# Kernel tuning notes

Hardware: AMD Instinct MI355X
Metric: run time of the kernel (lower is better)

The kernel has to match this reference:

```python
import jax, jax.numpy as jnp
import numpy as np

B, C, T = 32, 64, 512
K = 3            # period_channels / top-k frequencies
PMAX = T         # max period (== seq_len so output matches input length)
MIN_P = 32       # min_period_threshold
CMAX = T // MIN_P  # static upper bound on number of cycles
KERNELS = ((1, 1), (3, 3), (5, 5))


def _conv2d(x, w, b, pad):
    # x: [N, Cin, H, W], w: [Cout, Cin, kh, kw]
    y = jax.lax.conv_general_dilated(
        x, w, (1, 1), ((pad[0], pad[0]), (pad[1], pad[1])),
        dimension_numbers=('NCHW', 'OIHW', 'NCHW'))
    return y + b[None, :, None, None]


def _period_fold(seqs):
    # seqs: [BN, T]. FFT top-k period detection + gather-based fold into 2D grids.
    spec = jnp.fft.rfft(seqs, axis=-1)
    amp = jnp.abs(spec).at[..., 0].set(0.0)  # zero DC component
    vals, idx = jax.lax.top_k(amp, K)        # [BN, K]
    idx = jnp.maximum(idx, 1)
    P = jnp.clip(T // idx, MIN_P, PMAX)      # period length per branch
    cycles = jnp.maximum(T // P, 1)
    base = jnp.maximum(T - cycles * P, 0)    # start offset (keep trailing window)
    idx_c = jnp.arange(CMAX)
    idx_p = jnp.arange(PMAX)
    gidx = (base[:, :, None, None]
            + idx_c[None, None, :, None] * P[:, :, None, None]
            + idx_p[None, None, None, :])
    gidx = jnp.clip(gidx, 0, T - 1)          # [BN, K, CMAX, PMAX]
    gathered = seqs[jnp.arange(seqs.shape[0])[:, None, None, None], gidx]
    mask = ((idx_c[None, None, :, None] < cycles[:, :, None, None])
            & (idx_p[None, None, None, :] < P[:, :, None, None])).astype(seqs.dtype)
    return gathered * mask, mask, vals


def _forward(features, w_path0, b_path0, w_path1, b_path1, w_path2, b_path2,
             w_proj, b_proj, w_res, b_res, w_fuse, b_fuse):
    seqs = features.reshape(B * C, T)
    conv_in, mask, kamp = _period_fold(seqs)  # [B*C, K, CMAX, PMAX]
    # Inception block: parallel same-padded convs + 1x1 proj + residual 1x1 proj
    ws = (w_path0, w_path1, w_path2)
    bs = (b_path0, b_path1, b_path2)
    feats = [_conv2d(conv_in, w, b, (kh // 2, kw // 2))
             for w, b, (kh, kw) in zip(ws, bs, KERNELS)]
    z = _conv2d(jnp.concatenate(feats, axis=1), w_proj, b_proj, (0, 0))
    z = jax.nn.gelu(z, approximate=False)  # torch nn.GELU default = exact erf
    z2d = (z + _conv2d(conv_in, w_res, b_res, (0, 0))).reshape(B, C, CMAX, PMAX)
    mask5 = mask.reshape(B, C, K, CMAX, PMAX)
    conv_in5 = conv_in.reshape(B, C, K, CMAX, PMAX)
    eps = jnp.finfo(z2d.dtype).eps
    neg = jnp.finfo(z2d.dtype).min
    # masked avg / max pooling over cycles
    cycle_mask = mask5.max(axis=2)                       # [B,C,CMAX,PMAX]
    avg_pool = (z2d * cycle_mask).sum(axis=2) / (cycle_mask.sum(axis=2) + eps)
    valid = cycle_mask > 0
    max_pool = jnp.where(valid, z2d, neg).max(axis=2)
    max_pool = jnp.where(valid.any(axis=2), max_pool, 0.0)  # [B,C,PMAX]
    # amplitude-softmax weighted branch reconstruction back to 1D
    branch_sum = conv_in5.sum(axis=3)                    # [B,C,K,PMAX]
    branch_w = mask5.sum(axis=3)
    branch_recon = branch_sum / (branch_w + eps) * (branch_w > 0)
    branch_valid = mask5.max(axis=(3, 4)) > 0            # [B,C,K]
    amp = jnp.where(branch_valid, kamp.reshape(B, C, K), neg)
    bw = jax.nn.softmax(amp, axis=2) * branch_valid
    seq_recon = (branch_recon * bw[..., None]).sum(axis=2)  # [B,C,PMAX]
    combined = jnp.concatenate([avg_pool, max_pool, seq_recon], axis=1)  # [B,3C,PMAX]
    fused = jnp.einsum('oc,bct->bot', w_fuse, combined) + b_fuse[None, :, None]
    return jax.nn.gelu(fused, approximate=False)  # [B, C, T] residual update


def setup_inputs() -> dict:
    key = jax.random.key(0)
    ks = jax.random.split(key, 8)

    def conv_w(k, shape):
        fan_in = shape[1] * shape[2] * shape[3]
        return jax.random.normal(k, shape, jnp.float32) / float(np.sqrt(fan_in))

    inp = {'features': jax.random.normal(ks[0], (B, C, T), jnp.float32)}
    for i, (kh, kw) in enumerate(KERNELS):
        inp[f'w_path{i}'] = conv_w(ks[1 + i], (1, K, kh, kw))
        inp[f'b_path{i}'] = jnp.zeros((1,), jnp.float32)
    inp['w_proj'] = conv_w(ks[4], (1, len(KERNELS), 1, 1))
    inp['b_proj'] = jnp.zeros((1,), jnp.float32)
    inp['w_res'] = conv_w(ks[5], (1, K, 1, 1))
    inp['b_res'] = jnp.zeros((1,), jnp.float32)
    inp['w_fuse'] = jax.random.normal(ks[6], (C, 3 * C), jnp.float32) / float(np.sqrt(3 * C))
    inp['b_fuse'] = jnp.zeros((C,), jnp.float32)
    return inp


def reference(features, w_path0, b_path0, w_path1, b_path1, w_path2, b_path2,
              w_proj, b_proj, w_res, b_res, w_fuse, b_fuse):
    return _forward(features, w_path0, b_path0, w_path1, b_path1, w_path2, b_path2,
                    w_proj, b_proj, w_res, b_res, w_fuse, b_fuse)
```

## Files before the change

### kernel.cpp

```cpp
#include <hip/hip_runtime.h>
#include <math.h>

#define B_    32
#define C_    64
#define T_    512
#define NROWS (B_ * C_)
#define CMAX_ 16
#define FEPS  1.1920929e-07f

__device__ __forceinline__ float gelu_fast(float x) {
    float y = fmaf(0.044715f * x * x, x, x);
    float e = __builtin_exp2f(-2.3022808f * y);
    return x * __builtin_amdgcn_rcpf(1.0f + e);
}

__global__ __launch_bounds__(128) void mono_kernel(
    const float* __restrict__ feat,
    const float* __restrict__ w0, const float* __restrict__ b0,
    const float* __restrict__ w1, const float* __restrict__ b1,
    const float* __restrict__ w2, const float* __restrict__ b2,
    const float* __restrict__ wpj, const float* __restrict__ bpj,
    const float* __restrict__ wr, const float* __restrict__ br,
    float* __restrict__ avg_out, float* __restrict__ max_out,
    float* __restrict__ seq_out)
{
    __shared__ float rowp[1040];
    __shared__ __align__(16) float2 FA[256];
    __shared__ __align__(16) float2 FB[256];
    __shared__ float WeffS[80];
    __shared__ float wtopS[6];
    __shared__ int   itopS[6];
    __shared__ int   ipS[9];
    __shared__ float bwS[3];

    const int tid = threadIdx.x;
    const int r = blockIdx.x;

    {
        float4 v = reinterpret_cast<const float4*>(feat + (size_t)r * T_)[tid];
        int bi = 2 + tid * 4;
        rowp[bi + 0] = v.x; rowp[bi + 1] = v.y;
        rowp[bi + 2] = v.z; rowp[bi + 3] = v.w;
    }
    for (int i = 514 + tid; i < 1040; i += 128) rowp[i] = 0.f;
    if (tid == 0) { rowp[0] = 0.f; rowp[1] = 0.f; }
    if (tid < 80) {
        int i = tid;
        if (i < 75) {
            int k = i / 25, ij = i % 25, ii = ij / 5, jj = ij % 5;
            float w = wpj[2] * w2[k * 25 + ii * 5 + jj];
            if (ii >= 1 && ii <= 3 && jj >= 1 && jj <= 3)
                w += wpj[1] * w1[k * 9 + (ii - 1) * 3 + (jj - 1)];
            if (ii == 2 && jj == 2) w += wpj[0] * w0[k];
            WeffS[i] = w;
        } else if (i == 75) {
            WeffS[75] = wpj[0] * b0[0] + wpj[1] * b1[0] + wpj[2] * b2[0] + bpj[0];
        } else if (i <= 78) {
            WeffS[i] = wr[i - 76];
        } else {
            WeffS[79] = br[0];
        }
    }
    __syncthreads();

    FA[tid]       = make_float2(rowp[2 + 2 * tid],         rowp[2 + 2 * tid + 1]);
    FA[tid + 128] = make_float2(rowp[2 + 2 * (tid + 128)], rowp[2 + 2 * (tid + 128) + 1]);
    __syncthreads();

    {
        float2* src = FA;
        float2* dst = FB;
        #pragma unroll
        for (int s = 1; s <= 8; ++s) {
            const int l = 1 << (s - 1);
            const int p = tid & (l - 1);
            const int i0 = 2 * tid - p;
            const float rev = (float)p * (0.5f / (float)l);
            const float cw =  __builtin_amdgcn_cosf(rev);
            const float sw = -__builtin_amdgcn_sinf(rev);
            float2 a = src[tid];
            float2 b = src[tid + 128];
            float tr = cw * b.x - sw * b.y;
            float ti = cw * b.y + sw * b.x;
            dst[i0]     = make_float2(a.x + tr, a.y + ti);
            dst[i0 + l] = make_float2(a.x - tr, a.y - ti);
            __syncthreads();
            float2* tmp = src; src = dst; dst = tmp;
        }
    }

    float v[2]; int id[2];
    #pragma unroll
    for (int q = 0; q < 2; ++q) {
        const int k = 1 + tid + 128 * q;
        float2 A  = FA[k & 255];
        float2 Bv = FA[(256 - k) & 255];
        float Er = 0.5f * (A.x + Bv.x);
        float Ei = 0.5f * (A.y - Bv.y);
        float Or = 0.5f * (A.y + Bv.y);
        float Oi = 0.5f * (Bv.x - A.x);
        const float rev = (float)k * (1.0f / 512.0f);
        float sth = __builtin_amdgcn_sinf(rev);
        float cth = __builtin_amdgcn_cosf(rev);
        float Fr = Er + cth * Or + sth * Oi;
        float Fi = Ei + cth * Oi - sth * Or;
        v[q] = sqrtf(Fr * Fr + Fi * Fi);
        id[q] = k;
    }

    {
        const int wv = tid >> 6;
        float vals[3]; int idxs[3];
        #pragma unroll
        for (int kk = 0; kk < 3; ++kk) {
            float bv = v[0]; int bi = id[0];
            if (v[1] > bv || (v[1] == bv && id[1] < bi)) { bv = v[1]; bi = id[1]; }
            #pragma unroll
            for (int off = 32; off >= 1; off >>= 1) {
                float ov = __shfl_xor(bv, off, 64);
                int   oi = __shfl_xor(bi, off, 64);
                if (ov > bv || (ov == bv && oi < bi)) { bv = ov; bi = oi; }
            }
            vals[kk] = bv; idxs[kk] = bi;
            #pragma unroll
            for (int q = 0; q < 2; ++q)
                if (id[q] == bi) v[q] = -1e30f;
        }
        if ((tid & 63) == 0) {
            #pragma unroll
            for (int kk = 0; kk < 3; ++kk) {
                wtopS[wv * 3 + kk] = vals[kk];
                itopS[wv * 3 + kk] = idxs[kk];
            }
        }
    }
    __syncthreads();
    if (tid == 0) {
        float vv[6]; int ii[6];
        #pragma unroll
        for (int q = 0; q < 6; ++q) { vv[q] = wtopS[q]; ii[q] = itopS[q]; }
        float vals[3]; int idxs[3];
        #pragma unroll
        for (int kk = 0; kk < 3; ++kk) {
            float bv = vv[0]; int bi = ii[0];
            #pragma unroll
            for (int q = 1; q < 6; ++q)
                if (vv[q] > bv || (vv[q] == bv && ii[q] < bi)) { bv = vv[q]; bi = ii[q]; }
            vals[kk] = bv; idxs[kk] = bi;
            #pragma unroll
            for (int q = 0; q < 6; ++q)
                if (ii[q] == bi) vv[q] = -1e30f;
        }
        float m = fmaxf(vals[0], fmaxf(vals[1], vals[2]));
        float e0 = expf(vals[0] - m), e1 = expf(vals[1] - m), e2 = expf(vals[2] - m);
        float inv = 1.0f / (e0 + e1 + e2);
        bwS[0] = e0 * inv; bwS[1] = e1 * inv; bwS[2] = e2 * inv;
        #pragma unroll
        for (int kk = 0; kk < 3; ++kk) {
            int fi = idxs[kk];
            int P = T_ / fi;
            P = P < 32 ? 32 : (P > 512 ? 512 : P);
            int cyc = T_ / P;
            ipS[kk] = P; ipS[3 + kk] = cyc; ipS[6 + kk] = T_ - cyc * P;
        }
    }
    __syncthreads();

    const int P0  = __builtin_amdgcn_readfirstlane(ipS[0]);
    const int P1  = __builtin_amdgcn_readfirstlane(ipS[1]);
    const int P2  = __builtin_amdgcn_readfirstlane(ipS[2]);
    const int cy0 = __builtin_amdgcn_readfirstlane(ipS[3]);
    const int cy1 = __builtin_amdgcn_readfirstlane(ipS[4]);
    const int cy2 = __builtin_amdgcn_readfirstlane(ipS[5]);
    const int bs0 = __builtin_amdgcn_readfirstlane(ipS[6]);
    const int bs1 = __builtin_amdgcn_readfirstlane(ipS[7]);
    const int bs2 = __builtin_amdgcn_readfirstlane(ipS[8]);
    const float bw0 = bwS[0], bw1 = bwS[1], bw2 = bwS[2];
    const float beff = WeffS[75], wr0 = WeffS[76], wr1 = WeffS[77],
                wr2 = WeffS[78], bres = WeffS[79];

    int maxP = P0 > P1 ? P0 : P1; maxP = maxP > P2 ? maxP : P2;
    const int PkA[3]  = {P0, P1, P2};
    const int cykA[3] = {cy0, cy1, cy2};
    const int bskA[3] = {bs0, bs1, bs2};
    const int woff = tid & 64;

    #pragma unroll 1
    for (int pc = 0; pc < T_; pc += 128) {
        const int p = pc + tid;
        const int wb = __builtin_amdgcn_readfirstlane(pc + woff);
        if (wb >= maxP) {
            avg_out[r * T_ + p] = 0.f;
            max_out[r * T_ + p] = 0.f;
            seq_out[r * T_ + p] = 0.f;
            continue;
        }
        int c0 = (P0 > wb) ? cy0 : 0;
        int c1 = (P1 > wb) ? cy1 : 0;
        int c2 = (P2 > wb) ? cy2 : 0;
        int cymax = c0 > c1 ? c0 : c1; cymax = cymax > c2 ? cymax : c2;
        cymax = __builtin_amdgcn_readfirstlane(cymax);

        float zacc[CMAX_];
        #pragma unroll
        for (int i = 0; i < CMAX_; ++i) zacc[i] = beff;

        #pragma unroll 1
        for (int k = 0; k < 3; ++k) {
            const int P = PkA[k];
            if (wb >= P) continue;
            const int cy = cykA[k];
            const int bs = bskA[k];
            float Wk[5][5];
            #pragma unroll
            for (int i = 0; i < 5; ++i)
                #pragma unroll
                for (int j = 0; j < 5; ++j)
                    Wk[i][j] = WeffS[k * 25 + i * 5 + j];
            bool mdw[5];
            #pragma unroll
            for (int dw = -2; dw <= 2; ++dw)
                mdw[dw + 2] = ((unsigned)(p + dw) < (unsigned)P);
            const int base = bs + p;
            float cur[5], nxt[5];
            #pragma unroll
            for (int dw = 0; dw < 5; ++dw) { cur[dw] = rowp[base + dw]; nxt[dw] = 0.f; }
            #pragma unroll
            for (int hh = 0; hh < CMAX_; ++hh) {
                if (hh < cy) {
                    if (hh + 1 < cy) {
                        const int a = base + (hh + 1) * P;
                        #pragma unroll
                        for (int dw = 0; dw < 5; ++dw) nxt[dw] = rowp[a + dw];
                    }
                    float w[5];
                    #pragma unroll
                    for (int dw = 0; dw < 5; ++dw) w[dw] = mdw[dw] ? cur[dw] : 0.f;
                    #pragma unroll
                    for (int dh = -2; dh <= 2; ++dh) {
                        const int cc = hh - dh;
                        if (cc >= 0 && cc < CMAX_) {
                            #pragma unroll
                            for (int dw = 0; dw < 5; ++dw)
                                zacc[cc] = fmaf(Wk[dh + 2][dw], w[dw], zacc[cc]);
                        }
                    }
                    #pragma unroll
                    for (int dw = 0; dw < 5; ++dw) cur[dw] = nxt[dw];
                }
            }
        }

        float avg_num = 0.f, den = 0.f, mx = -3.402823466e38f;
        float s0 = 0.f, s1 = 0.f, s2 = 0.f;
        int anyv = 0;
        const int pl0 = (p < P0), pl1 = (p < P1), pl2 = (p < P2);
        #pragma unroll
        for (int cc = 0; cc < CMAX_; ++cc) {
            if (cc < cymax) {
                int m0 = (cc < cy0) & pl0;
                int m1 = (cc < cy1) & pl1;
                int m2 = (cc < cy2) & pl2;
                float x0v = m0 ? rowp[2 + bs0 + cc * P0 + p] : 0.f;
                float x1v = m1 ? rowp[2 + bs1 + cc * P1 + p] : 0.f;
                float x2v = m2 ? rowp[2 + bs2 + cc * P2 + p] : 0.f;
                float res = fmaf(wr0, x0v, fmaf(wr1, x1v, fmaf(wr2, x2v, bres)));
                float z = gelu_fast(zacc[cc]) + res;
                s0 += x0v; s1 += x1v; s2 += x2v;
                int mm = m0 | m1 | m2;
                float cm = mm ? 1.f : 0.f;
                avg_num += z * cm;
                den += cm;
                mx = mm ? fmaxf(mx, z) : mx;
                anyv |= mm;
            }
        }
        float avg = avg_num / (den + FEPS);
        float mpool = anyv ? mx : 0.f;

        float seq = 0.f;
        seq = fmaf(bw0, pl0 ? s0 / ((float)cy0 + FEPS) : 0.f, seq);
        seq = fmaf(bw1, pl1 ? s1 / ((float)cy1 + FEPS) : 0.f, seq);
        seq = fmaf(bw2, pl2 ? s2 / ((float)cy2 + FEPS) : 0.f, seq);

        avg_out[r * T_ + p] = avg;
        max_out[r * T_ + p] = mpool;
        seq_out[r * T_ + p] = seq;
    }
}

__global__ __launch_bounds__(256) void fuse_kernel(
    const float* __restrict__ avgb, const float* __restrict__ maxb,
    const float* __restrict__ seqb,
    const float* __restrict__ wf, const float* __restrict__ bfu,
    float* __restrict__ out)
{
    __shared__ float wT[64][70];
    __shared__ float Bt[64][40];
    const int tid = threadIdx.x;
    const int b = blockIdx.y;
    const int tt0 = blockIdx.x * 32;
    const int og = tid >> 3;
    const int tg = tid & 7;
    const int o0 = og * 2;
    const int t0 = tg * 4;

    float acc[2][4];
    #pragma unroll
    for (int i = 0; i < 2; ++i)
        #pragma unroll
        for (int j = 0; j < 4; ++j) acc[i][j] = 0.f;

    const float* srcs[3] = {avgb, maxb, seqb};
    for (int g = 0; g < 3; ++g) {
        const float* __restrict__ src = srcs[g];
        #pragma unroll
        for (int it = 0; it < 2; ++it) {
            int idx = tid + it * 256;
            int c = idx >> 3, t4 = idx & 7;
            float4 vv = reinterpret_cast<const float4*>(
                            &src[(b * 64 + c) * 512 + tt0])[t4];
            *reinterpret_cast<float4*>(&Bt[c][t4 * 4]) = vv;
        }
        #pragma unroll
        for (int it = 0; it < 16; ++it) {
            int i = tid + it * 256;
            int c = i & 63, o = i >> 6;
            wT[c][o] = wf[o * 192 + g * 64 + c];
        }
        __syncthreads();
        for (int c = 0; c < 64; ++c) {
            float2 wv = *reinterpret_cast<const float2*>(&wT[c][o0]);
            float4 bv = *reinterpret_cast<const float4*>(&Bt[c][t0]);
            const float wa[2] = {wv.x, wv.y};
            const float ba[4] = {bv.x, bv.y, bv.z, bv.w};
            #pragma unroll
            for (int i = 0; i < 2; ++i)
                #pragma unroll
                for (int j = 0; j < 4; ++j)
                    acc[i][j] = fmaf(wa[i], ba[j], acc[i][j]);
        }
        __syncthreads();
    }
    #pragma unroll
    for (int i = 0; i < 2; ++i) {
        float bias = bfu[o0 + i];
        float4 o4;
        o4.x = gelu_fast(acc[i][0] + bias);
        o4.y = gelu_fast(acc[i][1] + bias);
        o4.z = gelu_fast(acc[i][2] + bias);
        o4.w = gelu_fast(acc[i][3] + bias);
        *reinterpret_cast<float4*>(
            &out[(b * 64 + (o0 + i)) * 512 + tt0 + t0]) = o4;
    }
}

extern "C" void kernel_launch(void* const* d_in, const int* in_sizes, int n_in,
                              void* d_out, int out_size, void* d_ws, size_t ws_size,
                              hipStream_t stream) {
    const float* feat = (const float*)d_in[0];
    const float* w0  = (const float*)d_in[1];
    const float* b0  = (const float*)d_in[2];
    const float* w1  = (const float*)d_in[3];
    const float* b1  = (const float*)d_in[4];
    const float* w2  = (const float*)d_in[5];
    const float* b2  = (const float*)d_in[6];
    const float* wpj = (const float*)d_in[7];
    const float* bpj = (const float*)d_in[8];
    const float* wr  = (const float*)d_in[9];
    const float* br  = (const float*)d_in[10];
    const float* wf  = (const float*)d_in[11];
    const float* bfu = (const float*)d_in[12];

    float* ws = (float*)d_ws;
    float* avgb = ws;
    float* maxb = ws + (size_t)NROWS * T_;
    float* seqb = ws + 2 * (size_t)NROWS * T_;

    mono_kernel<<<NROWS, 128, 0, stream>>>(feat, w0, b0, w1, b1, w2, b2,
                                           wpj, bpj, wr, br, avgb, maxb, seqb);
    fuse_kernel<<<dim3(16, 32), 256, 0, stream>>>(avgb, maxb, seqb, wf, bfu,
                                                  (float*)d_out);
}
```

Baseline: 42.52 us.

## Split FFT into per-wavefront half-size transforms and unroll cycle loops in groups of four

Each wavefront now runs a 128-point FFT on the even or odd interleaved samples without block barriers between stages, and the two halves are combined in an extra radix-2 stage inside the spectrum magnitude computation. This removes eight block-wide __syncthreads from the FFT. The convolution and pooling loops over cycles are restructured into groups of four with clamped, branch-free shared-memory addresses, so loads can be issued ahead without register rotation. The cost is more complex twiddle math and redundant loads for masked-off cycles inside a group.

Result: faster. 41.11 us (-3.3%).

```diff
diff --git a/kernel.cpp b/kernel.cpp
--- a/kernel.cpp
+++ b/kernel.cpp
@@ -34,6 +34,8 @@
     __shared__ float bwS[3];
 
     const int tid = threadIdx.x;
+    const int lane = tid & 63;
+    const int wv = tid >> 6;
     const int r = blockIdx.x;
 
     {
@@ -63,53 +65,70 @@
     }
     __syncthreads();
 
-    FA[tid]       = make_float2(rowp[2 + 2 * tid],         rowp[2 + 2 * tid + 1]);
-    FA[tid + 128] = make_float2(rowp[2 + 2 * (tid + 128)], rowp[2 + 2 * (tid + 128) + 1]);
-    __syncthreads();
-
     {
-        float2* src = FA;
-        float2* dst = FB;
-        #pragma unroll
-        for (int s = 1; s <= 8; ++s) {
+        float2* Fw = FA + (wv << 7);
+        #pragma unroll
+        for (int n = lane; n < 128; n += 64)
+            Fw[n] = make_float2(rowp[2 + 4 * n + 2 * wv], rowp[3 + 4 * n + 2 * wv]);
+    }
+
+    {
+        float2* src = FA + (wv << 7);
+        float2* dst = FB + (wv << 7);
+        #pragma unroll
+        for (int s = 1; s <= 7; ++s) {
             const int l = 1 << (s - 1);
-            const int p = tid & (l - 1);
-            const int i0 = 2 * tid - p;
-            const float rev = (float)p * (0.5f / (float)l);
+            const int pl = lane & (l - 1);
+            const int i0 = 2 * lane - pl;
+            const float rev = (float)pl * (0.5f / (float)l);
             const float cw =  __builtin_amdgcn_cosf(rev);
             const float sw = -__builtin_amdgcn_sinf(rev);
-            float2 a = src[tid];
-            float2 b = src[tid + 128];
+            float2 a = src[lane];
+            float2 b = src[lane + 64];
             float tr = cw * b.x - sw * b.y;
             float ti = cw * b.y + sw * b.x;
             dst[i0]     = make_float2(a.x + tr, a.y + ti);
             dst[i0 + l] = make_float2(a.x - tr, a.y - ti);
-            __syncthreads();
             float2* tmp = src; src = dst; dst = tmp;
         }
     }
+    __syncthreads();
 
     float v[2]; int id[2];
-    #pragma unroll
-    for (int q = 0; q < 2; ++q) {
-        const int k = 1 + tid + 128 * q;
-        float2 A  = FA[k & 255];
-        float2 Bv = FA[(256 - k) & 255];
-        float Er = 0.5f * (A.x + Bv.x);
-        float Ei = 0.5f * (A.y - Bv.y);
-        float Or = 0.5f * (A.y + Bv.y);
-        float Oi = 0.5f * (Bv.x - A.x);
-        const float rev = (float)k * (1.0f / 512.0f);
-        float sth = __builtin_amdgcn_sinf(rev);
-        float cth = __builtin_amdgcn_cosf(rev);
-        float Fr = Er + cth * Or + sth * Oi;
-        float Fi = Ei + cth * Oi - sth * Or;
-        v[q] = sqrtf(Fr * Fr + Fi * Fi);
-        id[q] = k;
-    }
-
     {
-        const int wv = tid >> 6;
+        const float2* Fe = FB;
+        const float2* Fo = FB + 128;
+        const int k1 = tid + 1;
+        const int a = k1 & 127;
+        const int b = (128 - a) & 127;
+        float2 Fea = Fe[a], Foa = Fo[a], Feb = Fe[b], Fob = Fo[b];
+        const float revw = (float)k1 * (1.0f / 256.0f);
+        const float cw =  __builtin_amdgcn_cosf(revw);
+        const float sw = -__builtin_amdgcn_sinf(revw);
+        float wfr = cw * Foa.x - sw * Foa.y, wfi = cw * Foa.y + sw * Foa.x;
+        float cfr = cw * Fob.x + sw * Fob.y, cfi = cw * Fob.y - sw * Fob.x;
+        const float revu = (float)k1 * (1.0f / 512.0f);
+        const float su = __builtin_amdgcn_sinf(revu);
+        const float cu = __builtin_amdgcn_cosf(revu);
+        #pragma unroll
+        for (int q = 0; q < 2; ++q) {
+            const float sgn = q ? -1.f : 1.f;
+            float Ax = Fea.x + sgn * wfr, Ay = Fea.y + sgn * wfi;
+            float Bx = Feb.x + sgn * cfr, By = Feb.y + sgn * cfi;
+            float Er = 0.5f * (Ax + Bx);
+            float Ei = 0.5f * (Ay - By);
+            float Or = 0.5f * (Ay + By);
+            float Oi = 0.5f * (Bx - Ax);
+            float cth = q ? -su : cu;
+            float sth = q ?  cu : su;
+            float Fr = Er + cth * Or + sth * Oi;
+            float Fi = Ei + cth * Oi - sth * Or;
+            v[q] = sqrtf(Fr * Fr + Fi * Fi);
+            id[q] = k1 + 128 * q;
+        }
+    }
+
+    {
         float vals[3]; int idxs[3];
         #pragma unroll
         for (int kk = 0; kk < 3; ++kk) {
@@ -126,7 +145,7 @@
             for (int q = 0; q < 2; ++q)
                 if (id[q] == bi) v[q] = -1e30f;
         }
-        if ((tid & 63) == 0) {
+        if (lane == 0) {
             #pragma unroll
             for (int kk = 0; kk < 3; ++kk) {
                 wtopS[wv * 3 + kk] = vals[kk];
@@ -222,31 +241,29 @@
             for (int dw = -2; dw <= 2; ++dw)
                 mdw[dw + 2] = ((unsigned)(p + dw) < (unsigned)P);
             const int base = bs + p;
-            float cur[5], nxt[5];
-            #pragma unroll
-            for (int dw = 0; dw < 5; ++dw) { cur[dw] = rowp[base + dw]; nxt[dw] = 0.f; }
-            #pragma unroll
-            for (int hh = 0; hh < CMAX_; ++hh) {
-                if (hh < cy) {
-                    if (hh + 1 < cy) {
-                        const int a = base + (hh + 1) * P;
+            #pragma unroll
+            for (int g = 0; g < 4; ++g) {
+                if (4 * g < cy) {
+                    #pragma unroll
+                    for (int h4 = 0; h4 < 4; ++h4) {
+                        const int hh = 4 * g + h4;
+                        const int hoff = (hh < cy) ? 0 : 4096;
+                        int a0 = base + hh * P + hoff;
+                        a0 = a0 > 1031 ? 1031 : a0;
+                        float w[5];
                         #pragma unroll
-                        for (int dw = 0; dw < 5; ++dw) nxt[dw] = rowp[a + dw];
-                    }
-                    float w[5];
-                    #pragma unroll
-                    for (int dw = 0; dw < 5; ++dw) w[dw] = mdw[dw] ? cur[dw] : 0.f;
-                    #pragma unroll
-                    for (int dh = -2; dh <= 2; ++dh) {
-                        const int cc = hh - dh;
-                        if (cc >= 0 && cc < CMAX_) {
-                            #pragma unroll
-                            for (int dw = 0; dw < 5; ++dw)
-                                zacc[cc] = fmaf(Wk[dh + 2][dw], w[dw], zacc[cc]);
+                        for (int dw = 0; dw < 5; ++dw)
+                            w[dw] = mdw[dw] ? rowp[a0 + dw] : 0.f;
+                        #pragma unroll
+                        for (int dh = -2; dh <= 2; ++dh) {
+                            const int cc = hh - dh;
+                            if (cc >= 0 && cc < CMAX_) {
+                                #pragma unroll
+                                for (int dw = 0; dw < 5; ++dw)
+                                    zacc[cc] = fmaf(Wk[dh + 2][dw], w[dw], zacc[cc]);
+                            }
                         }
                     }
-                    #pragma unroll
-                    for (int dw = 0; dw < 5; ++dw) cur[dw] = nxt[dw];
                 }
             }
         }
@@ -256,23 +273,30 @@
         int anyv = 0;
         const int pl0 = (p < P0), pl1 = (p < P1), pl2 = (p < P2);
         #pragma unroll
-        for (int cc = 0; cc < CMAX_; ++cc) {
-            if (cc < cymax) {
-                int m0 = (cc < cy0) & pl0;
-                int m1 = (cc < cy1) & pl1;
-                int m2 = (cc < cy2) & pl2;
-                float x0v = m0 ? rowp[2 + bs0 + cc * P0 + p] : 0.f;
-                float x1v = m1 ? rowp[2 + bs1 + cc * P1 + p] : 0.f;
-                float x2v = m2 ? rowp[2 + bs2 + cc * P2 + p] : 0.f;
-                float res = fmaf(wr0, x0v, fmaf(wr1, x1v, fmaf(wr2, x2v, bres)));
-                float z = gelu_fast(zacc[cc]) + res;
-                s0 += x0v; s1 += x1v; s2 += x2v;
-                int mm = m0 | m1 | m2;
-                float cm = mm ? 1.f : 0.f;
-                avg_num += z * cm;
-                den += cm;
-                mx = mm ? fmaxf(mx, z) : mx;
-                anyv |= mm;
+        for (int cg = 0; cg < 4; ++cg) {
+            if (4 * cg < cymax) {
+                #pragma unroll
+                for (int c4 = 0; c4 < 4; ++c4) {
+                    const int cc = 4 * cg + c4;
+                    int m0 = (cc < cy0) & pl0;
+                    int m1 = (cc < cy1) & pl1;
+                    int m2 = (cc < cy2) & pl2;
+                    int a0 = 2 + bs0 + cc * P0 + p; a0 = a0 > 1036 ? 1036 : a0;
+                    int a1 = 2 + bs1 + cc * P1 + p; a1 = a1 > 1036 ? 1036 : a1;
+                    int a2 = 2 + bs2 + cc * P2 + p; a2 = a2 > 1036 ? 1036 : a2;
+                    float x0v = m0 ? rowp[a0] : 0.f;
+                    float x1v = m1 ? rowp[a1] : 0.f;
+                    float x2v = m2 ? rowp[a2] : 0.f;
+                    float res = fmaf(wr0, x0v, fmaf(wr1, x1v, fmaf(wr2, x2v, bres)));
+                    float z = gelu_fast(zacc[cc]) + res;
+                    s0 += x0v; s1 += x1v; s2 += x2v;
+                    int mm = m0 | m1 | m2;
+                    float cm = mm ? 1.f : 0.f;
+                    avg_num += z * cm;
+                    den += cm;
+                    mx = mm ? fmaxf(mx, z) : mx;
+                    anyv |= mm;
+                }
             }
         }
         float avg = avg_num / (den + FEPS);
```

## Use single-wavefront blocks, drop barriers, merge conv weights when periods match

Applied to the files above, without the earlier changes.

The per-row kernel now runs with 64 threads, one wavefront, per block, with each thread handling twice as many FFT butterflies and output positions. This removes every __syncthreads and the two-stage cross-wave top-k that went through shared memory. The top-k result now stays in registers, read with readfirstlane. When all three detected periods are equal, the three conv branches share one folded grid, so their 5x5 weights are pre-summed and the conv runs once instead of three times. The conv row loop also drops its register prefetch and uses clamped shared-memory addresses. The cost is less parallelism inside each block, and the code now relies on in-wave ordering of shared-memory accesses instead of explicit barriers.

Result: slower. 43.83 us (+3.1%).

```diff
diff --git a/kernel.cpp b/kernel.cpp
--- a/kernel.cpp
+++ b/kernel.cpp
@@ -14,7 +14,7 @@
     return x * __builtin_amdgcn_rcpf(1.0f + e);
 }
 
-__global__ __launch_bounds__(128) void mono_kernel(
+__global__ __launch_bounds__(64) void mono_kernel(
     const float* __restrict__ feat,
     const float* __restrict__ w0, const float* __restrict__ b0,
     const float* __restrict__ w1, const float* __restrict__ b1,
@@ -28,24 +28,22 @@
     __shared__ __align__(16) float2 FA[256];
     __shared__ __align__(16) float2 FB[256];
     __shared__ float WeffS[80];
-    __shared__ float wtopS[6];
-    __shared__ int   itopS[6];
-    __shared__ int   ipS[9];
-    __shared__ float bwS[3];
+    __shared__ float WsumS[25];
 
     const int tid = threadIdx.x;
     const int r = blockIdx.x;
 
     {
-        float4 v = reinterpret_cast<const float4*>(feat + (size_t)r * T_)[tid];
-        int bi = 2 + tid * 4;
-        rowp[bi + 0] = v.x; rowp[bi + 1] = v.y;
-        rowp[bi + 2] = v.z; rowp[bi + 3] = v.w;
-    }
-    for (int i = 514 + tid; i < 1040; i += 128) rowp[i] = 0.f;
-    if (tid == 0) { rowp[0] = 0.f; rowp[1] = 0.f; }
-    if (tid < 80) {
-        int i = tid;
+        const float4* f4 = reinterpret_cast<const float4*>(feat + (size_t)r * T_);
+        float4 v0 = f4[tid], v1 = f4[tid + 64];
+        const int b0i = 2 + tid * 4, b1i = 2 + (tid + 64) * 4;
+        rowp[b0i] = v0.x; rowp[b0i + 1] = v0.y; rowp[b0i + 2] = v0.z; rowp[b0i + 3] = v0.w;
+        rowp[b1i] = v1.x; rowp[b1i + 1] = v1.y; rowp[b1i + 2] = v1.z; rowp[b1i + 3] = v1.w;
+    }
+    for (int i = 514 + tid; i < 1040; i += 64) rowp[i] = 0.f;
+    if (tid < 2) rowp[tid] = 0.f;
+
+    for (int i = tid; i < 80; i += 64) {
         if (i < 75) {
             int k = i / 25, ij = i % 25, ii = ij / 5, jj = ij % 5;
             float w = wpj[2] * w2[k * 25 + ii * 5 + jj];
@@ -61,11 +59,13 @@
             WeffS[79] = br[0];
         }
     }
-    __syncthreads();
-
-    FA[tid]       = make_float2(rowp[2 + 2 * tid],         rowp[2 + 2 * tid + 1]);
-    FA[tid + 128] = make_float2(rowp[2 + 2 * (tid + 128)], rowp[2 + 2 * (tid + 128) + 1]);
-    __syncthreads();
+    if (tid < 25) WsumS[tid] = WeffS[tid] + WeffS[25 + tid] + WeffS[50 + tid];
+
+    #pragma unroll
+    for (int q = 0; q < 4; ++q) {
+        const int n = tid + (q << 6);
+        FA[n] = make_float2(rowp[2 + 2 * n], rowp[3 + 2 * n]);
+    }
 
     {
         float2* src = FA;
@@ -73,26 +73,29 @@
         #pragma unroll
         for (int s = 1; s <= 8; ++s) {
             const int l = 1 << (s - 1);
-            const int p = tid & (l - 1);
-            const int i0 = 2 * tid - p;
-            const float rev = (float)p * (0.5f / (float)l);
-            const float cw =  __builtin_amdgcn_cosf(rev);
-            const float sw = -__builtin_amdgcn_sinf(rev);
-            float2 a = src[tid];
-            float2 b = src[tid + 128];
-            float tr = cw * b.x - sw * b.y;
-            float ti = cw * b.y + sw * b.x;
-            dst[i0]     = make_float2(a.x + tr, a.y + ti);
-            dst[i0 + l] = make_float2(a.x - tr, a.y - ti);
-            __syncthreads();
-            float2* tmp = src; src = dst; dst = tmp;
-        }
-    }
-
-    float v[2]; int id[2];
-    #pragma unroll
-    for (int q = 0; q < 2; ++q) {
-        const int k = 1 + tid + 128 * q;
+            #pragma unroll
+            for (int h = 0; h < 2; ++h) {
+                const int j = tid + (h << 6);
+                const int pl = j & (l - 1);
+                const int i0 = 2 * j - pl;
+                const float rev = (float)pl * (0.5f / (float)l);
+                const float cw =  __builtin_amdgcn_cosf(rev);
+                const float sw = -__builtin_amdgcn_sinf(rev);
+                float2 a = src[j];
+                float2 b = src[j + 128];
+                float tr = cw * b.x - sw * b.y;
+                float ti = cw * b.y + sw * b.x;
+                dst[i0]     = make_float2(a.x + tr, a.y + ti);
+                dst[i0 + l] = make_float2(a.x - tr, a.y - ti);
+            }
+            float2* t = src; src = dst; dst = t;
+        }
+    }
+
+    float v[4]; int id[4];
+    #pragma unroll
+    for (int q = 0; q < 4; ++q) {
+        const int k = 1 + tid + (q << 6);
         float2 A  = FA[k & 255];
         float2 Bv = FA[(256 - k) & 255];
         float Er = 0.5f * (A.x + Bv.x);
@@ -108,145 +111,120 @@
         id[q] = k;
     }
 
+    float vals[3]; int idxs[3];
+    #pragma unroll
+    for (int kk = 0; kk < 3; ++kk) {
+        float bv = v[0]; int bi = id[0];
+        #pragma unroll
+        for (int q = 1; q < 4; ++q)
+            if (v[q] > bv || (v[q] == bv && id[q] < bi)) { bv = v[q]; bi = id[q]; }
+        #pragma unroll
+        for (int off = 32; off >= 1; off >>= 1) {
+            float ov = __shfl_xor(bv, off, 64);
+            int   oi = __shfl_xor(bi, off, 64);
+            if (ov > bv || (ov == bv && oi < bi)) { bv = ov; bi = oi; }
+        }
+        vals[kk] = bv; idxs[kk] = bi;
+        #pragma unroll
+        for (int q = 0; q < 4; ++q)
+            if (id[q] == bi) v[q] = -1e30f;
+    }
+
+    float bw0, bw1, bw2;
+    int P_[3], cy_[3], bs_[3];
     {
-        const int wv = tid >> 6;
-        float vals[3]; int idxs[3];
-        #pragma unroll
-        for (int kk = 0; kk < 3; ++kk) {
-            float bv = v[0]; int bi = id[0];
-            if (v[1] > bv || (v[1] == bv && id[1] < bi)) { bv = v[1]; bi = id[1]; }
-            #pragma unroll
-            for (int off = 32; off >= 1; off >>= 1) {
-                float ov = __shfl_xor(bv, off, 64);
-                int   oi = __shfl_xor(bi, off, 64);
-                if (ov > bv || (ov == bv && oi < bi)) { bv = ov; bi = oi; }
-            }
-            vals[kk] = bv; idxs[kk] = bi;
-            #pragma unroll
-            for (int q = 0; q < 2; ++q)
-                if (id[q] == bi) v[q] = -1e30f;
-        }
-        if ((tid & 63) == 0) {
-            #pragma unroll
-            for (int kk = 0; kk < 3; ++kk) {
-                wtopS[wv * 3 + kk] = vals[kk];
-                itopS[wv * 3 + kk] = idxs[kk];
-            }
-        }
-    }
-    __syncthreads();
-    if (tid == 0) {
-        float vv[6]; int ii[6];
-        #pragma unroll
-        for (int q = 0; q < 6; ++q) { vv[q] = wtopS[q]; ii[q] = itopS[q]; }
-        float vals[3]; int idxs[3];
-        #pragma unroll
-        for (int kk = 0; kk < 3; ++kk) {
-            float bv = vv[0]; int bi = ii[0];
-            #pragma unroll
-            for (int q = 1; q < 6; ++q)
-                if (vv[q] > bv || (vv[q] == bv && ii[q] < bi)) { bv = vv[q]; bi = ii[q]; }
-            vals[kk] = bv; idxs[kk] = bi;
-            #pragma unroll
-            for (int q = 0; q < 6; ++q)
-                if (ii[q] == bi) vv[q] = -1e30f;
-        }
         float m = fmaxf(vals[0], fmaxf(vals[1], vals[2]));
         float e0 = expf(vals[0] - m), e1 = expf(vals[1] - m), e2 = expf(vals[2] - m);
         float inv = 1.0f / (e0 + e1 + e2);
-        bwS[0] = e0 * inv; bwS[1] = e1 * inv; bwS[2] = e2 * inv;
+        bw0 = e0 * inv; bw1 = e1 * inv; bw2 = e2 * inv;
         #pragma unroll
         for (int kk = 0; kk < 3; ++kk) {
             int fi = idxs[kk];
             int P = T_ / fi;
             P = P < 32 ? 32 : (P > 512 ? 512 : P);
             int cyc = T_ / P;
-            ipS[kk] = P; ipS[3 + kk] = cyc; ipS[6 + kk] = T_ - cyc * P;
-        }
-    }
-    __syncthreads();
-
-    const int P0  = __builtin_amdgcn_readfirstlane(ipS[0]);
-    const int P1  = __builtin_amdgcn_readfirstlane(ipS[1]);
-    const int P2  = __builtin_amdgcn_readfirstlane(ipS[2]);
-    const int cy0 = __builtin_amdgcn_readfirstlane(ipS[3]);
-    const int cy1 = __builtin_amdgcn_readfirstlane(ipS[4]);
-    const int cy2 = __builtin_amdgcn_readfirstlane(ipS[5]);
-    const int bs0 = __builtin_amdgcn_readfirstlane(ipS[6]);
-    const int bs1 = __builtin_amdgcn_readfirstlane(ipS[7]);
-    const int bs2 = __builtin_amdgcn_readfirstlane(ipS[8]);
-    const float bw0 = bwS[0], bw1 = bwS[1], bw2 = bwS[2];
+            P_[kk] = P; cy_[kk] = cyc; bs_[kk] = T_ - cyc * P;
+        }
+    }
+    const int P0  = __builtin_amdgcn_readfirstlane(P_[0]);
+    const int P1  = __builtin_amdgcn_readfirstlane(P_[1]);
+    const int P2  = __builtin_amdgcn_readfirstlane(P_[2]);
+    const int cy0 = __builtin_amdgcn_readfirstlane(cy_[0]);
+    const int cy1 = __builtin_amdgcn_readfirstlane(cy_[1]);
+    const int cy2 = __builtin_amdgcn_readfirstlane(cy_[2]);
+    const int bs0 = __builtin_amdgcn_readfirstlane(bs_[0]);
+    const int bs1 = __builtin_amdgcn_readfirstlane(bs_[1]);
+    const int bs2 = __builtin_amdgcn_readfirstlane(bs_[2]);
     const float beff = WeffS[75], wr0 = WeffS[76], wr1 = WeffS[77],
                 wr2 = WeffS[78], bres = WeffS[79];
 
     int maxP = P0 > P1 ? P0 : P1; maxP = maxP > P2 ? maxP : P2;
+    const bool fastp = (P0 == P1) && (P1 == P2);
+    const int kcount = fastp ? 1 : 3;
     const int PkA[3]  = {P0, P1, P2};
     const int cykA[3] = {cy0, cy1, cy2};
     const int bskA[3] = {bs0, bs1, bs2};
-    const int woff = tid & 64;
+    const size_t rT = (size_t)r * T_;
 
     #pragma unroll 1
-    for (int pc = 0; pc < T_; pc += 128) {
+    for (int pc = 0; pc < T_; pc += 64) {
         const int p = pc + tid;
-        const int wb = __builtin_amdgcn_readfirstlane(pc + woff);
-        if (wb >= maxP) {
-            avg_out[r * T_ + p] = 0.f;
-            max_out[r * T_ + p] = 0.f;
-            seq_out[r * T_ + p] = 0.f;
+        if (pc >= maxP) {
+            avg_out[rT + p] = 0.f;
+            max_out[rT + p] = 0.f;
+            seq_out[rT + p] = 0.f;
             continue;
         }
-        int c0 = (P0 > wb) ? cy0 : 0;
-        int c1 = (P1 > wb) ? cy1 : 0;
-        int c2 = (P2 > wb) ? cy2 : 0;
+        int c0 = (P0 > pc) ? cy0 : 0;
+        int c1 = (P1 > pc) ? cy1 : 0;
+        int c2 = (P2 > pc) ? cy2 : 0;
         int cymax = c0 > c1 ? c0 : c1; cymax = cymax > c2 ? cymax : c2;
-        cymax = __builtin_amdgcn_readfirstlane(cymax);
 
         float zacc[CMAX_];
         #pragma unroll
         for (int i = 0; i < CMAX_; ++i) zacc[i] = beff;
 
         #pragma unroll 1
-        for (int k = 0; k < 3; ++k) {
+        for (int k = 0; k < kcount; ++k) {
             const int P = PkA[k];
-            if (wb >= P) continue;
+            if (pc >= P) continue;
             const int cy = cykA[k];
             const int bs = bskA[k];
+            const float* Wsrc = fastp ? WsumS : (WeffS + k * 25);
             float Wk[5][5];
             #pragma unroll
             for (int i = 0; i < 5; ++i)
                 #pragma unroll
                 for (int j = 0; j < 5; ++j)
-                    Wk[i][j] = WeffS[k * 25 + i * 5 + j];
+                    Wk[i][j] = Wsrc[i * 5 + j];
             bool mdw[5];
             #pragma unroll
             for (int dw = -2; dw <= 2; ++dw)
                 mdw[dw + 2] = ((unsigned)(p + dw) < (unsigned)P);
             const int base = bs + p;
-            float cur[5], nxt[5];
-            #pragma unroll
-            for (int dw = 0; dw < 5; ++dw) { cur[dw] = rowp[base + dw]; nxt[dw] = 0.f; }
-            #pragma unroll
-            for (int hh = 0; hh < CMAX_; ++hh) {
-                if (hh < cy) {
-                    if (hh + 1 < cy) {
-                        const int a = base + (hh + 1) * P;
+            #pragma unroll
+            for (int g = 0; g < 4; ++g) {
+                if (4 * g < cy) {
+                    #pragma unroll
+                    for (int h4 = 0; h4 < 4; ++h4) {
+                        const int hh = 4 * g + h4;
+                        const int hoff = (hh < cy) ? 0 : 4096;
+                        int a0 = base + hh * P + hoff;
+                        a0 = a0 > 1031 ? 1031 : a0;
+                        float w[5];
                         #pragma unroll
-                        for (int dw = 0; dw < 5; ++dw) nxt[dw] = rowp[a + dw];
-                    }
-                    float w[5];
-                    #pragma unroll
-                    for (int dw = 0; dw < 5; ++dw) w[dw] = mdw[dw] ? cur[dw] : 0.f;
-                    #pragma unroll
-                    for (int dh = -2; dh <= 2; ++dh) {
-                        const int cc = hh - dh;
-                        if (cc >= 0 && cc < CMAX_) {
-                            #pragma unroll
-                            for (int dw = 0; dw < 5; ++dw)
-                                zacc[cc] = fmaf(Wk[dh + 2][dw], w[dw], zacc[cc]);
+                        for (int dw = 0; dw < 5; ++dw)
+                            w[dw] = mdw[dw] ? rowp[a0 + dw] : 0.f;
+                        #pragma unroll
+                        for (int dh = -2; dh <= 2; ++dh) {
+                            const int cc = hh - dh;
+                            if (cc >= 0 && cc < CMAX_) {
+                                #pragma unroll
+                                for (int dw = 0; dw < 5; ++dw)
+                                    zacc[cc] = fmaf(Wk[dh + 2][dw], w[dw], zacc[cc]);
+                            }
                         }
                     }
-                    #pragma unroll
-                    for (int dw = 0; dw < 5; ++dw) cur[dw] = nxt[dw];
                 }
             }
         }
@@ -256,23 +234,30 @@
         int anyv = 0;
         const int pl0 = (p < P0), pl1 = (p < P1), pl2 = (p < P2);
         #pragma unroll
-        for (int cc = 0; cc < CMAX_; ++cc) {
-            if (cc < cymax) {
-                int m0 = (cc < cy0) & pl0;
-                int m1 = (cc < cy1) & pl1;
-                int m2 = (cc < cy2) & pl2;
-                float x0v = m0 ? rowp[2 + bs0 + cc * P0 + p] : 0.f;
-                float x1v = m1 ? rowp[2 + bs1 + cc * P1 + p] : 0.f;
-                float x2v = m2 ? rowp[2 + bs2 + cc * P2 + p] : 0.f;
-                float res = fmaf(wr0, x0v, fmaf(wr1, x1v, fmaf(wr2, x2v, bres)));
-                float z = gelu_fast(zacc[cc]) + res;
-                s0 += x0v; s1 += x1v; s2 += x2v;
-                int mm = m0 | m1 | m2;
-                float cm = mm ? 1.f : 0.f;
-                avg_num += z * cm;
-                den += cm;
-                mx = mm ? fmaxf(mx, z) : mx;
-                anyv |= mm;
+        for (int cg = 0; cg < 4; ++cg) {
+            if (4 * cg < cymax) {
+                #pragma unroll
+                for (int c4 = 0; c4 < 4; ++c4) {
+                    const int cc = 4 * cg + c4;
+                    int m0 = (cc < cy0) & pl0;
+                    int m1 = (cc < cy1) & pl1;
+                    int m2 = (cc < cy2) & pl2;
+                    int a0 = 2 + bs0 + cc * P0 + p; a0 = a0 > 1036 ? 1036 : a0;
+                    int a1 = 2 + bs1 + cc * P1 + p; a1 = a1 > 1036 ? 1036 : a1;
+                    int a2 = 2 + bs2 + cc * P2 + p; a2 = a2 > 1036 ? 1036 : a2;
+                    float x0v = m0 ? rowp[a0] : 0.f;
+                    float x1v = m1 ? rowp[a1] : 0.f;
+                    float x2v = m2 ? rowp[a2] : 0.f;
+                    float res = fmaf(wr0, x0v, fmaf(wr1, x1v, fmaf(wr2, x2v, bres)));
+                    float z = gelu_fast(zacc[cc]) + res;
+                    s0 += x0v; s1 += x1v; s2 += x2v;
+                    int mm = m0 | m1 | m2;
+                    float cm = mm ? 1.f : 0.f;
+                    avg_num += z * cm;
+                    den += cm;
+                    mx = mm ? fmaxf(mx, z) : mx;
+                    anyv |= mm;
+                }
             }
         }
         float avg = avg_num / (den + FEPS);
@@ -283,9 +268,9 @@
         seq = fmaf(bw1, pl1 ? s1 / ((float)cy1 + FEPS) : 0.f, seq);
         seq = fmaf(bw2, pl2 ? s2 / ((float)cy2 + FEPS) : 0.f, seq);
 
-        avg_out[r * T_ + p] = avg;
-        max_out[r * T_ + p] = mpool;
-        seq_out[r * T_ + p] = seq;
+        avg_out[rT + p] = avg;
+        max_out[rT + p] = mpool;
+        seq_out[rT + p] = seq;
     }
 }
 
@@ -377,8 +362,8 @@
     float* maxb = ws + (size_t)NROWS * T_;
     float* seqb = ws + 2 * (size_t)NROWS * T_;
 
-    mono_kernel<<<NROWS, 128, 0, stream>>>(feat, w0, b0, w1, b1, w2, b2,
-                                           wpj, bpj, wr, br, avgb, maxb, seqb);
+    mono_kernel<<<NROWS, 64, 0, stream>>>(feat, w0, b0, w1, b1, w2, b2,
+                                          wpj, bpj, wr, br, avgb, maxb, seqb);
     fuse_kernel<<<dim3(16, 32), 256, 0, stream>>>(avgb, maxb, seqb, wf, bfu,
                                                   (float*)d_out);
 }
```
